# Kernel optimization log

Hardware: AMD Instinct MI355X
Metric: run time of the kernel (lower is better)

The kernel has to match this reference:

```python
import jax, jax.numpy as jnp
import numpy as np

N_NODES = 50000
N_EDGES = 800000
H_DIM = 128
N_REL = 40
N_BASES = 4


def setup_inputs() -> dict:
    key = jax.random.key(0)
    ks = jax.random.split(key, 9)
    h = jax.random.normal(ks[0], (N_NODES, H_DIM), jnp.float32)
    norm = jax.random.uniform(ks[1], (N_EDGES, 1), jnp.float32)
    basis_w = jax.random.normal(ks[2], (N_BASES, H_DIM, H_DIM), jnp.float32) * 0.05
    w_comp = jax.random.normal(ks[3], (N_REL, N_BASES), jnp.float32) * 0.5
    loop_w = jax.random.normal(ks[4], (H_DIM, H_DIM), jnp.float32) * 0.05
    bias = jax.random.normal(ks[5], (H_DIM,), jnp.float32) * 0.05
    src = jax.random.randint(ks[6], (N_EDGES,), 0, N_NODES, jnp.int32)
    dst = jax.random.randint(ks[7], (N_EDGES,), 0, N_NODES, jnp.int32)
    etype = jax.random.randint(ks[8], (N_EDGES,), 0, N_REL, jnp.int32)
    return {"h": h, "norm": norm, "basis_w": basis_w, "w_comp": w_comp,
            "loop_w": loop_w, "bias": bias, "src": src, "dst": dst, "etype": etype}


def reference(h, norm, basis_w, w_comp, loop_w, bias, src, dst, etype):
    # RelGraphConv with 'basis' regularizer, one layer (num_hidden_layers=1):
    #   W_r = sum_b w_comp[r, b] * basis_w[b]
    #   m_e = (h[src_e] @ W_{etype_e}) * norm_e
    #   agg[v] = sum_{e: dst_e = v} m_e
    #   out = relu(agg + bias + h @ loop_w)   (dropout = 0)
    # Contraction reordered for memory efficiency: scatter-add per-basis
    # scaled source features first (node-level), then apply small basis GEMMs.
    n = h.shape[0]
    n_bases = basis_w.shape[0]
    coeff = w_comp[etype] * norm          # [E, B] per-edge basis coefficients * norm
    h_src = h[src]                        # [E, D] edge-gathered source features
    agg = jnp.zeros((n, basis_w.shape[2]), dtype=h.dtype)
    for b in range(n_bases):              # small fixed loop over bases
        s_b = jax.ops.segment_sum(coeff[:, b:b + 1] * h_src, dst, num_segments=n)  # [N, D]
        agg = agg + s_b @ basis_w[b]
    return jax.nn.relu(agg + bias + h @ loop_w)
```

## Files before the change

### kernel.cpp

```cpp
#include <hip/hip_runtime.h>
#include <hip/hip_bf16.h>
#include <stdint.h>

#define N_NODES 50000
#define N_EDGES 800000
#define H_DIM 128
#define N_REL 40
#define N_BASES 4
#define A_COLS 640
#define N_RANGES 196
#define EP_BLOCKS 200
#define EDGES_PER_BLK 4000
#define STAGE_CAP 5120

typedef __attribute__((ext_vector_type(8))) short bf16x8;
typedef __attribute__((ext_vector_type(4))) float f32x4;

__device__ __forceinline__ unsigned short f2bf(float f) {
    unsigned int u = __float_as_uint(f);
    unsigned int r = u + 0x7fffu + ((u >> 16) & 1u);
    return (unsigned short)(r >> 16);
}

__global__ __launch_bounds__(256) void prep_kernel(
        const float* __restrict__ h,
        const float* __restrict__ basis_w, const float* __restrict__ loop_w,
        const int* __restrict__ src, const int* __restrict__ dst,
        const int* __restrict__ etype, const float* __restrict__ norm,
        unsigned short* __restrict__ A, unsigned short* __restrict__ wt3,
        uint2* __restrict__ pkd, int* __restrict__ gcnt) {
    int bid = blockIdx.x;
    if (bid < 3125) {
        int t = bid * 256 + threadIdx.x;
        int row = t >> 4;
        int cb = (t & 15) * 8;
        const float* p = h + (size_t)row * 128 + cb;
        float4 a0 = ((const float4*)p)[0];
        float4 a1 = ((const float4*)p)[1];
        bf16x8 o;
        o[0] = (short)f2bf(a0.x); o[1] = (short)f2bf(a0.y);
        o[2] = (short)f2bf(a0.z); o[3] = (short)f2bf(a0.w);
        o[4] = (short)f2bf(a1.x); o[5] = (short)f2bf(a1.y);
        o[6] = (short)f2bf(a1.z); o[7] = (short)f2bf(a1.w);
        *(bf16x8*)(A + (size_t)row * A_COLS + cb) = o;
    } else if (bid < 3130) {
        int mat = bid - 3125;
        const float* srcm = (mat < 4) ? (basis_w + mat * 16384) : loop_w;
        int koff = (mat < 4) ? (128 + mat * 128) : 0;
        int t = threadIdx.x;
#pragma unroll
        for (int i = 0; i < 16; ++i) {
            int f = t + i * 256;
            int k = f >> 5;
            int j4 = (f & 31) * 4;
            float4 v = ((const float4*)srcm)[f];
            int kg = koff + k;
            int ks = kg >> 5;
            int quad = (kg >> 3) & 3;
            int jj = kg & 7;
            float vv[4] = {v.x, v.y, v.z, v.w};
#pragma unroll
            for (int d = 0; d < 4; ++d) {
                int j = j4 + d;
                int cg = j >> 4;
                int n16 = j & 15;
                wt3[(size_t)((ks * 8 + cg) * 64 + quad * 16 + n16) * 8 + jj] =
                    f2bf(vv[d]);
            }
        }
    } else {
        __shared__ int lhist[N_RANGES];
        int blk = bid - 3130;
        int t = threadIdx.x;
        if (t < N_RANGES) lhist[t] = 0;
        __syncthreads();
        int e0 = blk * EDGES_PER_BLK;
        for (int i = t; i < EDGES_PER_BLK; i += 256) {
            int e = e0 + i;
            int d = dst[e];
            unsigned int nbf = f2bf(norm[e]);
            pkd[e] = make_uint2((unsigned)src[e] | ((unsigned)etype[e] << 20),
                                (unsigned)d | (nbf << 17));
            atomicAdd(&lhist[d >> 8], 1);
        }
        __syncthreads();
        if (t < N_RANGES) gcnt[t * EP_BLOCKS + blk] = lhist[t];
    }
}

__global__ __launch_bounds__(256) void bucket_scan_a(
        const int* __restrict__ gcnt, int* __restrict__ blkbase,
        int* __restrict__ btot) {
    __shared__ int wsum[4];
    int r = blockIdx.x;
    int t = threadIdx.x, lane = t & 63, w = t >> 6;
    int x = (t < EP_BLOCKS) ? gcnt[r * EP_BLOCKS + t] : 0;
    int v = x;
#pragma unroll
    for (int d = 1; d < 64; d <<= 1) {
        int y = __shfl_up(v, d);
        if (lane >= d) v += y;
    }
    if (lane == 63) wsum[w] = v;
    __syncthreads();
    int wpre = 0;
    if (w > 0) wpre += wsum[0];
    if (w > 1) wpre += wsum[1];
    if (w > 2) wpre += wsum[2];
    if (t < EP_BLOCKS) blkbase[r * EP_BLOCKS + t] = wpre + v - x;
    if (t == 255) btot[r] = wpre + v;
}

__global__ __launch_bounds__(256) void bucket_scan_b(
        const int* __restrict__ btot, int* __restrict__ bstart,
        int* __restrict__ offs) {
    __shared__ int wsum[4];
    int t = threadIdx.x, lane = t & 63, w = t >> 6;
    int x = (t < N_RANGES) ? btot[t] : 0;
    int v = x;
#pragma unroll
    for (int d = 1; d < 64; d <<= 1) {
        int y = __shfl_up(v, d);
        if (lane >= d) v += y;
    }
    if (lane == 63) wsum[w] = v;
    __syncthreads();
    int wpre = 0;
    if (w > 0) wpre += wsum[0];
    if (w > 1) wpre += wsum[1];
    if (w > 2) wpre += wsum[2];
    if (t < N_RANGES) bstart[t] = wpre + v - x;
    if (t == 255) {
        bstart[N_RANGES] = wpre + v;
        offs[N_NODES] = wpre + v;
    }
}

__global__ __launch_bounds__(256) void binscatter(
        const uint2* __restrict__ pkd, const int* __restrict__ blkbase,
        const int* __restrict__ bstart, uint2* __restrict__ bucketed) {
    __shared__ int lcur[N_RANGES];
    int t = threadIdx.x;
    if (t < N_RANGES)
        lcur[t] = bstart[t] + blkbase[t * EP_BLOCKS + blockIdx.x];
    __syncthreads();
    int e0 = blockIdx.x * EDGES_PER_BLK;
    for (int i = t; i < EDGES_PER_BLK; i += 256) {
        uint2 p = pkd[e0 + i];
        int r = (p.y & 0x1FFFF) >> 8;
        int pos = atomicAdd(&lcur[r], 1);
        bucketed[pos] = p;
    }
}

__global__ __launch_bounds__(256) void bucket_sort(
        const int* __restrict__ bstart, const uint2* __restrict__ bucketed,
        uint2* __restrict__ sorted_pe, int* __restrict__ offs) {
    __shared__ int hist[256];
    __shared__ int cur[256];
    __shared__ int wsum[4];
    __shared__ uint2 stage[STAGE_CAP];
    int r = blockIdx.x;
    int t = threadIdx.x, lane = t & 63, w = t >> 6;
    int begin = bstart[r];
    int end = bstart[r + 1];
    int n = end - begin;
    hist[t] = 0;
    __syncthreads();
    for (int i = begin + t; i < end; i += 256)
        atomicAdd(&hist[bucketed[i].y & 255], 1);
    __syncthreads();
    int x = hist[t];
    int v = x;
#pragma unroll
    for (int d = 1; d < 64; d <<= 1) {
        int y = __shfl_up(v, d);
        if (lane >= d) v += y;
    }
    if (lane == 63) wsum[w] = v;
    __syncthreads();
    int wpre = 0;
    if (w > 0) wpre += wsum[0];
    if (w > 1) wpre += wsum[1];
    if (w > 2) wpre += wsum[2];
    int excl_rel = wpre + v - x;
    int node = r * 256 + t;
    if (node < N_NODES) offs[node] = begin + excl_rel;
    cur[t] = excl_rel;
    __syncthreads();
    if (n <= STAGE_CAP) {
        for (int i = begin + t; i < end; i += 256) {
            uint2 p = bucketed[i];
            int pos = atomicAdd(&cur[p.y & 255], 1);
            stage[pos] = make_uint2(p.x, (p.y >> 17) << 16);
        }
        __syncthreads();
        for (int i = t; i < n; i += 256)
            sorted_pe[begin + i] = stage[i];
    } else {
        for (int i = begin + t; i < end; i += 256) {
            uint2 p = bucketed[i];
            int pos = atomicAdd(&cur[p.y & 255], 1);
            sorted_pe[begin + pos] = make_uint2(p.x, (p.y >> 17) << 16);
        }
    }
}

__global__ __launch_bounds__(256) void aggregate_kernel(
        const int* __restrict__ offs, const uint2* __restrict__ sorted_pe,
        const float* __restrict__ w_comp,
        unsigned short* __restrict__ A) {
    int v = __builtin_amdgcn_readfirstlane(blockIdx.x * 4 + (threadIdx.x >> 6));
    if (v >= N_NODES) return;
    int lane = threadIdx.x & 63;
    int begin = offs[v];
    int end = offs[v + 1];

    float a0l = 0.f, a0h = 0.f, a1l = 0.f, a1h = 0.f;
    float a2l = 0.f, a2h = 0.f, a3l = 0.f, a3h = 0.f;

    const unsigned int* Au = (const unsigned int*)A;

    int j = begin;
    for (; j + 8 <= end; j += 8) {
        uint2 p[8];
        unsigned int u[8];
#pragma unroll
        for (int q = 0; q < 8; ++q) p[q] = sorted_pe[j + q];
#pragma unroll
        for (int q = 0; q < 8; ++q)
            u[q] = Au[(size_t)(p[q].x & 0xFFFFF) * 320 + lane];
#pragma unroll
        for (int q = 0; q < 8; ++q) {
            float4 wc = ((const float4*)w_comp)[p[q].x >> 20];
            float nm = __uint_as_float(p[q].y);
            float lo = __uint_as_float(u[q] << 16);
            float hi = __uint_as_float(u[q] & 0xffff0000u);
            a0l += (wc.x * nm) * lo; a0h += (wc.x * nm) * hi;
            a1l += (wc.y * nm) * lo; a1h += (wc.y * nm) * hi;
            a2l += (wc.z * nm) * lo; a2h += (wc.z * nm) * hi;
            a3l += (wc.w * nm) * lo; a3h += (wc.w * nm) * hi;
        }
    }
    for (; j < end; ++j) {
        uint2 p = sorted_pe[j];
        int s = p.x & 0xFFFFF;
        float4 wc = ((const float4*)w_comp)[p.x >> 20];
        float nm = __uint_as_float(p.y);
        unsigned int u = Au[(size_t)s * 320 + lane];
        float lo = __uint_as_float(u << 16);
        float hi = __uint_as_float(u & 0xffff0000u);
        a0l += (wc.x * nm) * lo; a0h += (wc.x * nm) * hi;
        a1l += (wc.y * nm) * lo; a1h += (wc.y * nm) * hi;
        a2l += (wc.z * nm) * lo; a2h += (wc.z * nm) * hi;
        a3l += (wc.w * nm) * lo; a3h += (wc.w * nm) * hi;
    }

    unsigned int* ps = (unsigned int*)(A + (size_t)v * A_COLS + 128);
    ps[0 * 64 + lane] = (unsigned int)f2bf(a0l) | ((unsigned int)f2bf(a0h) << 16);
    ps[1 * 64 + lane] = (unsigned int)f2bf(a1l) | ((unsigned int)f2bf(a1h) << 16);
    ps[2 * 64 + lane] = (unsigned int)f2bf(a2l) | ((unsigned int)f2bf(a2h) << 16);
    ps[3 * 64 + lane] = (unsigned int)f2bf(a3l) | ((unsigned int)f2bf(a3h) << 16);
}

__global__ __launch_bounds__(256, 2) void gemm_out(
        const unsigned short* __restrict__ A,
        const unsigned short* __restrict__ wt3,
        const float* __restrict__ bias,
        float* __restrict__ out) {
    int wv = threadIdx.x >> 6;
    int lane = threadIdx.x & 63;
    int n16 = lane & 15;
    int quad = lane >> 4;
    int r0 = (blockIdx.x * 4 + wv) * 32;

    const unsigned short* ap0 = A + (size_t)(r0 + n16) * A_COLS + quad * 8;
    const unsigned short* ap1 = ap0 + 16 * A_COLS;
    const unsigned short* bp = wt3 + (size_t)lane * 8;

    f32x4 acc[2][8];
#pragma unroll
    for (int rt = 0; rt < 2; ++rt)
#pragma unroll
        for (int ct = 0; ct < 8; ++ct)
            acc[rt][ct] = (f32x4)0.f;

    bf16x8 a_cur[2], b_cur[8];
    a_cur[0] = *(const bf16x8*)ap0;
    a_cur[1] = *(const bf16x8*)ap1;
#pragma unroll
    for (int ct = 0; ct < 8; ++ct)
        b_cur[ct] = *(const bf16x8*)(bp + ct * 512);

#pragma unroll
    for (int ks = 0; ks < 20; ++ks) {
        bf16x8 a_nxt[2], b_nxt[8];
        if (ks < 19) {
            a_nxt[0] = *(const bf16x8*)(ap0 + (ks + 1) * 32);
            a_nxt[1] = *(const bf16x8*)(ap1 + (ks + 1) * 32);
#pragma unroll
            for (int ct = 0; ct < 8; ++ct)
                b_nxt[ct] = *(const bf16x8*)(bp + (ks + 1) * 4096 + ct * 512);
        } else {
            a_nxt[0] = a_cur[0];
            a_nxt[1] = a_cur[1];
#pragma unroll
            for (int ct = 0; ct < 8; ++ct) b_nxt[ct] = b_cur[ct];
        }
#pragma unroll
        for (int ct = 0; ct < 8; ++ct) {
            acc[0][ct] = __builtin_amdgcn_mfma_f32_16x16x32_bf16(a_cur[0], b_cur[ct], acc[0][ct], 0, 0, 0);
            acc[1][ct] = __builtin_amdgcn_mfma_f32_16x16x32_bf16(a_cur[1], b_cur[ct], acc[1][ct], 0, 0, 0);
        }
        a_cur[0] = a_nxt[0];
        a_cur[1] = a_nxt[1];
#pragma unroll
        for (int ct = 0; ct < 8; ++ct) b_cur[ct] = b_nxt[ct];
    }

#pragma unroll
    for (int rt = 0; rt < 2; ++rt) {
        int rbase = r0 + rt * 16 + quad * 4;
#pragma unroll
        for (int ct = 0; ct < 8; ++ct) {
            int col = ct * 16 + n16;
            float bv = bias[col];
#pragma unroll
            for (int rg = 0; rg < 4; ++rg) {
                int r = rbase + rg;
                if (r < N_NODES)
                    out[(size_t)r * H_DIM + col] = fmaxf(acc[rt][ct][rg] + bv, 0.f);
            }
        }
    }
}

extern "C" void kernel_launch(void* const* d_in, const int* in_sizes, int n_in,
                              void* d_out, int out_size, void* d_ws, size_t ws_size,
                              hipStream_t stream) {
    const float* h       = (const float*)d_in[0];
    const float* norm    = (const float*)d_in[1];
    const float* basis_w = (const float*)d_in[2];
    const float* w_comp  = (const float*)d_in[3];
    const float* loop_w  = (const float*)d_in[4];
    const float* bias    = (const float*)d_in[5];
    const int*   src     = (const int*)d_in[6];
    const int*   dst     = (const int*)d_in[7];
    const int*   etype   = (const int*)d_in[8];
    float* out = (float*)d_out;

    char* base = (char*)d_ws;
    unsigned short* wt3       = (unsigned short*)(base + 0);
    unsigned short* A         = (unsigned short*)(base + 163840);
    int*            offs      = (int*)(base + 64225280);
    uint2*          pkd       = (uint2*)(base + 64425344);
    uint2*          bucketed  = (uint2*)(base + 70825344);
    uint2*          sorted_pe = (uint2*)(base + 77225344);
    int*            gcnt      = (int*)(base + 83625344);
    int*            blkbase   = (int*)(base + 83782144);
    int*            bstart    = (int*)(base + 83938944);
    int*            btot      = (int*)(base + 83939732);

    prep_kernel<<<3330, 256, 0, stream>>>(h, basis_w, loop_w,
                                          src, dst, etype, norm,
                                          A, wt3, pkd, gcnt);
    bucket_scan_a<<<N_RANGES, 256, 0, stream>>>(gcnt, blkbase, btot);
    bucket_scan_b<<<1, 256, 0, stream>>>(btot, bstart, offs);
    binscatter<<<EP_BLOCKS, 256, 0, stream>>>(pkd, blkbase, bstart, bucketed);
    bucket_sort<<<N_RANGES, 256, 0, stream>>>(bstart, bucketed, sorted_pe, offs);
    aggregate_kernel<<<12500, 256, 0, stream>>>(offs, sorted_pe, w_comp, A);
    gemm_out<<<391, 256, 0, stream>>>(A, wt3, bias, out);
}
```

Measured before the change: 198.7 us.

## Merge bucket scans, split aggregate wave into edge halves, shrink GEMM blocks

The two bucket-scan launches are merged into one launch: an extra block recomputes the per-range totals directly and scans them, which removes a kernel boundary. The aggregate kernel now has each half-wave process a different edge, with 8-byte gathers per lane, and the two halves are combined by a cross-half shuffle before storing. This doubles gather width per lane and halves the serial edge loop per node, at the cost of more accumulators and a shuffle reduction. The output GEMM is relaunched as 64-thread single-wave blocks, four times as many, for finer-grained scheduling.

```diff
diff --git a/kernel.cpp b/kernel.cpp
--- a/kernel.cpp
+++ b/kernel.cpp
@@ -88,51 +88,51 @@
     }
 }
 
-__global__ __launch_bounds__(256) void bucket_scan_a(
+__global__ __launch_bounds__(256) void bucket_scan(
         const int* __restrict__ gcnt, int* __restrict__ blkbase,
-        int* __restrict__ btot) {
+        int* __restrict__ bstart, int* __restrict__ offs) {
     __shared__ int wsum[4];
     int r = blockIdx.x;
     int t = threadIdx.x, lane = t & 63, w = t >> 6;
-    int x = (t < EP_BLOCKS) ? gcnt[r * EP_BLOCKS + t] : 0;
-    int v = x;
-#pragma unroll
-    for (int d = 1; d < 64; d <<= 1) {
-        int y = __shfl_up(v, d);
-        if (lane >= d) v += y;
-    }
-    if (lane == 63) wsum[w] = v;
-    __syncthreads();
-    int wpre = 0;
-    if (w > 0) wpre += wsum[0];
-    if (w > 1) wpre += wsum[1];
-    if (w > 2) wpre += wsum[2];
-    if (t < EP_BLOCKS) blkbase[r * EP_BLOCKS + t] = wpre + v - x;
-    if (t == 255) btot[r] = wpre + v;
-}
-
-__global__ __launch_bounds__(256) void bucket_scan_b(
-        const int* __restrict__ btot, int* __restrict__ bstart,
-        int* __restrict__ offs) {
-    __shared__ int wsum[4];
-    int t = threadIdx.x, lane = t & 63, w = t >> 6;
-    int x = (t < N_RANGES) ? btot[t] : 0;
-    int v = x;
-#pragma unroll
-    for (int d = 1; d < 64; d <<= 1) {
-        int y = __shfl_up(v, d);
-        if (lane >= d) v += y;
-    }
-    if (lane == 63) wsum[w] = v;
-    __syncthreads();
-    int wpre = 0;
-    if (w > 0) wpre += wsum[0];
-    if (w > 1) wpre += wsum[1];
-    if (w > 2) wpre += wsum[2];
-    if (t < N_RANGES) bstart[t] = wpre + v - x;
-    if (t == 255) {
-        bstart[N_RANGES] = wpre + v;
-        offs[N_NODES] = wpre + v;
+    if (r < N_RANGES) {
+        int x = (t < EP_BLOCKS) ? gcnt[r * EP_BLOCKS + t] : 0;
+        int v = x;
+#pragma unroll
+        for (int d = 1; d < 64; d <<= 1) {
+            int y = __shfl_up(v, d);
+            if (lane >= d) v += y;
+        }
+        if (lane == 63) wsum[w] = v;
+        __syncthreads();
+        int wpre = 0;
+        if (w > 0) wpre += wsum[0];
+        if (w > 1) wpre += wsum[1];
+        if (w > 2) wpre += wsum[2];
+        if (t < EP_BLOCKS) blkbase[r * EP_BLOCKS + t] = wpre + v - x;
+    } else {
+        int tot = 0;
+        if (t < N_RANGES) {
+            const int* row = gcnt + t * EP_BLOCKS;
+#pragma unroll 8
+            for (int b = 0; b < EP_BLOCKS; ++b) tot += row[b];
+        }
+        int v = tot;
+#pragma unroll
+        for (int d = 1; d < 64; d <<= 1) {
+            int y = __shfl_up(v, d);
+            if (lane >= d) v += y;
+        }
+        if (lane == 63) wsum[w] = v;
+        __syncthreads();
+        int wpre = 0;
+        if (w > 0) wpre += wsum[0];
+        if (w > 1) wpre += wsum[1];
+        if (w > 2) wpre += wsum[2];
+        if (t < N_RANGES) bstart[t] = wpre + v - tot;
+        if (t == 255) {
+            bstart[N_RANGES] = wpre + v;
+            offs[N_NODES] = wpre + v;
+        }
     }
 }
 
@@ -213,66 +213,117 @@
     int v = __builtin_amdgcn_readfirstlane(blockIdx.x * 4 + (threadIdx.x >> 6));
     if (v >= N_NODES) return;
     int lane = threadIdx.x & 63;
+    int half = lane >> 5;
+    int m = lane & 31;
     int begin = offs[v];
     int end = offs[v + 1];
 
-    float a0l = 0.f, a0h = 0.f, a1l = 0.f, a1h = 0.f;
-    float a2l = 0.f, a2h = 0.f, a3l = 0.f, a3h = 0.f;
-
-    const unsigned int* Au = (const unsigned int*)A;
+    float acc[4][4];
+#pragma unroll
+    for (int b = 0; b < 4; ++b)
+#pragma unroll
+        for (int k = 0; k < 4; ++k) acc[b][k] = 0.f;
+
+    const uint2* Au2 = (const uint2*)A;
+    const float4* wcv = (const float4*)w_comp;
 
     int j = begin;
     for (; j + 8 <= end; j += 8) {
         uint2 p[8];
-        unsigned int u[8];
 #pragma unroll
         for (int q = 0; q < 8; ++q) p[q] = sorted_pe[j + q];
-#pragma unroll
-        for (int q = 0; q < 8; ++q)
-            u[q] = Au[(size_t)(p[q].x & 0xFFFFF) * 320 + lane];
-#pragma unroll
-        for (int q = 0; q < 8; ++q) {
-            float4 wc = ((const float4*)w_comp)[p[q].x >> 20];
-            float nm = __uint_as_float(p[q].y);
-            float lo = __uint_as_float(u[q] << 16);
-            float hi = __uint_as_float(u[q] & 0xffff0000u);
-            a0l += (wc.x * nm) * lo; a0h += (wc.x * nm) * hi;
-            a1l += (wc.y * nm) * lo; a1h += (wc.y * nm) * hi;
-            a2l += (wc.z * nm) * lo; a2h += (wc.z * nm) * hi;
-            a3l += (wc.w * nm) * lo; a3h += (wc.w * nm) * hi;
-        }
-    }
-    for (; j < end; ++j) {
-        uint2 p = sorted_pe[j];
-        int s = p.x & 0xFFFFF;
-        float4 wc = ((const float4*)w_comp)[p.x >> 20];
-        float nm = __uint_as_float(p.y);
-        unsigned int u = Au[(size_t)s * 320 + lane];
-        float lo = __uint_as_float(u << 16);
-        float hi = __uint_as_float(u & 0xffff0000u);
-        a0l += (wc.x * nm) * lo; a0h += (wc.x * nm) * hi;
-        a1l += (wc.y * nm) * lo; a1h += (wc.y * nm) * hi;
-        a2l += (wc.z * nm) * lo; a2h += (wc.z * nm) * hi;
-        a3l += (wc.w * nm) * lo; a3h += (wc.w * nm) * hi;
-    }
-
-    unsigned int* ps = (unsigned int*)(A + (size_t)v * A_COLS + 128);
-    ps[0 * 64 + lane] = (unsigned int)f2bf(a0l) | ((unsigned int)f2bf(a0h) << 16);
-    ps[1 * 64 + lane] = (unsigned int)f2bf(a1l) | ((unsigned int)f2bf(a1h) << 16);
-    ps[2 * 64 + lane] = (unsigned int)f2bf(a2l) | ((unsigned int)f2bf(a2h) << 16);
-    ps[3 * 64 + lane] = (unsigned int)f2bf(a3l) | ((unsigned int)f2bf(a3h) << 16);
-}
-
-__global__ __launch_bounds__(256, 2) void gemm_out(
+        uint2 u[4];
+#pragma unroll
+        for (int q = 0; q < 4; ++q) {
+            int sa = p[2 * q].x & 0xFFFFF;
+            int sb = p[2 * q + 1].x & 0xFFFFF;
+            int ss = half ? sb : sa;
+            u[q] = Au2[(size_t)ss * 160 + m];
+        }
+#pragma unroll
+        for (int q = 0; q < 4; ++q) {
+            float4 wa = wcv[p[2 * q].x >> 20];
+            float4 wb = wcv[p[2 * q + 1].x >> 20];
+            float na = __uint_as_float(p[2 * q].y);
+            float nb = __uint_as_float(p[2 * q + 1].y);
+            float4 wsel = half ? wb : wa;
+            float nsel = half ? nb : na;
+            float c0 = wsel.x * nsel, c1 = wsel.y * nsel;
+            float c2 = wsel.z * nsel, c3 = wsel.w * nsel;
+            float l0 = __uint_as_float(u[q].x << 16);
+            float h0 = __uint_as_float(u[q].x & 0xffff0000u);
+            float l1 = __uint_as_float(u[q].y << 16);
+            float h1 = __uint_as_float(u[q].y & 0xffff0000u);
+            acc[0][0] += c0 * l0; acc[0][1] += c0 * h0; acc[0][2] += c0 * l1; acc[0][3] += c0 * h1;
+            acc[1][0] += c1 * l0; acc[1][1] += c1 * h0; acc[1][2] += c1 * l1; acc[1][3] += c1 * h1;
+            acc[2][0] += c2 * l0; acc[2][1] += c2 * h0; acc[2][2] += c2 * l1; acc[2][3] += c2 * h1;
+            acc[3][0] += c3 * l0; acc[3][1] += c3 * h0; acc[3][2] += c3 * l1; acc[3][3] += c3 * h1;
+        }
+    }
+    for (; j + 2 <= end; j += 2) {
+        uint2 p0 = sorted_pe[j], p1 = sorted_pe[j + 1];
+        int sa = p0.x & 0xFFFFF, sb = p1.x & 0xFFFFF;
+        int ss = half ? sb : sa;
+        uint2 u = Au2[(size_t)ss * 160 + m];
+        float4 wa = wcv[p0.x >> 20], wb = wcv[p1.x >> 20];
+        float na = __uint_as_float(p0.y), nb = __uint_as_float(p1.y);
+        float4 wsel = half ? wb : wa;
+        float nsel = half ? nb : na;
+        float c0 = wsel.x * nsel, c1 = wsel.y * nsel;
+        float c2 = wsel.z * nsel, c3 = wsel.w * nsel;
+        float l0 = __uint_as_float(u.x << 16);
+        float h0 = __uint_as_float(u.x & 0xffff0000u);
+        float l1 = __uint_as_float(u.y << 16);
+        float h1 = __uint_as_float(u.y & 0xffff0000u);
+        acc[0][0] += c0 * l0; acc[0][1] += c0 * h0; acc[0][2] += c0 * l1; acc[0][3] += c0 * h1;
+        acc[1][0] += c1 * l0; acc[1][1] += c1 * h0; acc[1][2] += c1 * l1; acc[1][3] += c1 * h1;
+        acc[2][0] += c2 * l0; acc[2][1] += c2 * h0; acc[2][2] += c2 * l1; acc[2][3] += c2 * h1;
+        acc[3][0] += c3 * l0; acc[3][1] += c3 * h0; acc[3][2] += c3 * l1; acc[3][3] += c3 * h1;
+    }
+    if (j < end) {
+        uint2 p0 = sorted_pe[j];
+        int ss = p0.x & 0xFFFFF;
+        uint2 u = Au2[(size_t)ss * 160 + m];
+        float4 wa = wcv[p0.x >> 20];
+        float nsel = half ? 0.f : __uint_as_float(p0.y);
+        float c0 = wa.x * nsel, c1 = wa.y * nsel;
+        float c2 = wa.z * nsel, c3 = wa.w * nsel;
+        float l0 = __uint_as_float(u.x << 16);
+        float h0 = __uint_as_float(u.x & 0xffff0000u);
+        float l1 = __uint_as_float(u.y << 16);
+        float h1 = __uint_as_float(u.y & 0xffff0000u);
+        acc[0][0] += c0 * l0; acc[0][1] += c0 * h0; acc[0][2] += c0 * l1; acc[0][3] += c0 * h1;
+        acc[1][0] += c1 * l0; acc[1][1] += c1 * h0; acc[1][2] += c1 * l1; acc[1][3] += c1 * h1;
+        acc[2][0] += c2 * l0; acc[2][1] += c2 * h0; acc[2][2] += c2 * l1; acc[2][3] += c2 * h1;
+        acc[3][0] += c3 * l0; acc[3][1] += c3 * h0; acc[3][2] += c3 * l1; acc[3][3] += c3 * h1;
+    }
+
+#pragma unroll
+    for (int b = 0; b < 4; ++b)
+#pragma unroll
+        for (int k = 0; k < 4; ++k)
+            acc[b][k] += __shfl_xor(acc[b][k], 32);
+
+    uint2* ps2 = (uint2*)A + (size_t)v * 160 + 32;
+#pragma unroll
+    for (int bb = 0; bb < 2; ++bb) {
+        int b = half * 2 + bb;
+        uint2 o;
+        o.x = (unsigned int)f2bf(acc[b][0]) | ((unsigned int)f2bf(acc[b][1]) << 16);
+        o.y = (unsigned int)f2bf(acc[b][2]) | ((unsigned int)f2bf(acc[b][3]) << 16);
+        ps2[b * 32 + m] = o;
+    }
+}
+
+__global__ __launch_bounds__(64) void gemm_out(
         const unsigned short* __restrict__ A,
         const unsigned short* __restrict__ wt3,
         const float* __restrict__ bias,
         float* __restrict__ out) {
-    int wv = threadIdx.x >> 6;
-    int lane = threadIdx.x & 63;
+    int lane = threadIdx.x;
     int n16 = lane & 15;
     int quad = lane >> 4;
-    int r0 = (blockIdx.x * 4 + wv) * 32;
+    int r0 = blockIdx.x * 32;
 
     const unsigned short* ap0 = A + (size_t)(r0 + n16) * A_COLS + quad * 8;
     const unsigned short* ap1 = ap0 + 16 * A_COLS;
@@ -359,15 +410,13 @@
     int*            gcnt      = (int*)(base + 83625344);
     int*            blkbase   = (int*)(base + 83782144);
     int*            bstart    = (int*)(base + 83938944);
-    int*            btot      = (int*)(base + 83939732);
 
     prep_kernel<<<3330, 256, 0, stream>>>(h, basis_w, loop_w,
                                           src, dst, etype, norm,
                                           A, wt3, pkd, gcnt);
-    bucket_scan_a<<<N_RANGES, 256, 0, stream>>>(gcnt, blkbase, btot);
-    bucket_scan_b<<<1, 256, 0, stream>>>(btot, bstart, offs);
+    bucket_scan<<<N_RANGES + 1, 256, 0, stream>>>(gcnt, blkbase, bstart, offs);
     binscatter<<<EP_BLOCKS, 256, 0, stream>>>(pkd, blkbase, bstart, bucketed);
     bucket_sort<<<N_RANGES, 256, 0, stream>>>(bstart, bucketed, sorted_pe, offs);
     aggregate_kernel<<<12500, 256, 0, stream>>>(offs, sorted_pe, w_comp, A);
-    gemm_out<<<391, 256, 0, stream>>>(A, wt3, bias, out);
-}
+    gemm_out<<<1564, 64, 0, stream>>>(A, wt3, bias, out);
+}
```

Result: slower. 233.5 us (+17.5%).
